# Performance work log

Measured on AMD Instinct MI355X. Metric: run time of the kernel, lower is better.

The kernel has to match this reference:

```python
import jax, jax.numpy as jnp
import numpy as np

# SOM hyperparameters (from init_kwargs)
M_ROWS = 64
N_COLS = 64
DIM = 256
MAX_EPOCHS = 100
INITIAL_RADIUS = 32.0  # max(m, n) / 2
INITIAL_LR = 0.1
STD_COEFF = 0.5
BATCH = 8192

# [m*n, 2] integer grid locations (constant, non-differentiable)
_LOC_VECTS = jnp.asarray(
    np.stack(np.meshgrid(np.arange(M_ROWS), np.arange(N_COLS), indexing='ij'), axis=-1).reshape(-1, 2),
    dtype=jnp.int32,
)


def setup_inputs() -> dict:
    key = jax.random.key(0)
    k1, k2 = jax.random.split(key)
    return {
        'input_vect': jax.random.normal(k1, (BATCH, DIM), dtype=jnp.float32),
        'weights': jax.random.normal(k2, (M_ROWS * N_COLS, DIM), dtype=jnp.float32),
        'epoch': 10,
    }


def reference(input_vect, weights, epoch):
    # squared_distance[b, m] = sum_d (weights[m, d] - x[b, d])^2  -> [B, M]
    sq_dist = (
        jnp.sum(input_vect * input_vect, axis=1, keepdims=True)
        - 2.0 * (input_vect @ weights.T)
        + jnp.sum(weights * weights, axis=1)[None, :]
    )
    bmu_indices = jnp.argmin(sq_dist, axis=1)             # [B]
    bmu_locs = _LOC_VECTS[bmu_indices]                    # [B, 2]

    ep = jnp.float32(epoch)
    radius = INITIAL_RADIUS - ep * ((INITIAL_RADIUS - 1.0) / (MAX_EPOCHS - 1.0))
    alpha = INITIAL_LR * (1.0 - ep / MAX_EPOCHS)

    # bmu_distance_squares[b, m] = ||locs[m] - bmu_locs[b]||^2  -> [B, M]
    diff = _LOC_VECTS[None, :, :] - bmu_locs[:, None, :]  # int [B, M, 2]
    bmu_dist_sq = jnp.sum(diff * diff, axis=2).astype(jnp.float32)

    denom_nf = 2.0 * jnp.square(radius * STD_COEFF)
    learning_rate_op = jnp.exp(-bmu_dist_sq / denom_nf) * alpha  # [B, M]

    # numerator[m, d] = sum_b lr[b, m] * x[b, d]
    numerator = jnp.einsum('bm,bd->md', learning_rate_op, input_vect)
    denominator = jnp.sum(learning_rate_op, axis=0)[:, None] + 1e-12  # [M, 1]
    new_weights = numerator / denominator
    return bmu_locs, new_weights
```

## Files before the change

### kernel.cpp

```cpp
#include <hip/hip_runtime.h>
#include <stdint.h>

#define DIM   256
#define BATCH 8192
#define MCELL 4096

typedef unsigned long long u64;
typedef unsigned short u16;
typedef __attribute__((ext_vector_type(8))) short bf16x8;
typedef __attribute__((ext_vector_type(4))) float f32x4;

__device__ __forceinline__ u64 packMin(float v, unsigned idx) {
    unsigned u = __float_as_uint(v);
    u = (u & 0x80000000u) ? ~u : (u | 0x80000000u);
    return ((u64)u << 32) | (u64)idx;
}
__device__ __forceinline__ u16 f2bf(float f) {
    unsigned u = __float_as_uint(f);
    u += 0x7fffu + ((u >> 16) & 1u);
    return (u16)(u >> 16);
}
__device__ __forceinline__ void gll16(const void* g, const char* l) {
    __builtin_amdgcn_global_load_lds(
        (const __attribute__((address_space(1))) unsigned int*)g,
        (__attribute__((address_space(3))) unsigned int*)l, 16, 0, 0);
}
__device__ __forceinline__ u64 umin64(u64 a, u64 b) { return a < b ? a : b; }
__device__ __forceinline__ u64 umax64(u64 a, u64 b) { return a < b ? b : a; }
__device__ __forceinline__ void ins2(u64& t1, u64& t2, u64 p) {
    u64 hi = umax64(p, t1);
    t1 = umin64(p, t1);
    t2 = umin64(t2, hi);
}
__device__ __forceinline__ void merge2(u64& a1, u64& a2, u64 o1, u64 o2) {
    u64 H1 = umax64(a1, o1);
    a1 = umin64(a1, o1);
    a2 = umin64(H1, umin64(a2, o2));
}
__device__ __forceinline__ void merge3(u64& a1, u64& a2, u64& a3,
                                       u64 o1, u64 o2, u64 o3) {
    u64 L1 = umin64(a1, o1), H1 = umax64(a1, o1);
    u64 L2 = umin64(a2, o2);
    u64 L3 = umin64(a3, o3);
    a1 = L1;
    a2 = umin64(H1, L2);
    a3 = umin64(umax64(H1, L2), L3);
}

__global__ void k_prep(const float* __restrict__ X, const float* __restrict__ W,
                       u16* __restrict__ Xh, u16* __restrict__ Wh,
                       float* __restrict__ w2, const int* __restrict__ epoch_p,
                       float* __restrict__ scal) {
    const int blk = blockIdx.x;
    const int t = threadIdx.x;
    if (blk == 3072) {
        int raw = epoch_p[0];
        float ep = (raw >= 0 && raw < 100000) ? (float)raw : __int_as_float(raw);
        float radius = 32.0f - ep * (31.0f / 99.0f);
        float alpha  = 0.1f * (1.0f - ep / 100.0f);
        float rs = radius * 0.5f;
        float denom = 2.0f * rs * rs;
        if (t < 64)       scal[t]  = expf(-((float)(t * t)) / denom);
        else if (t == 64) scal[64] = alpha;
        return;
    }
    if (blk < 2048) {
        const int fi = blk * 256 + t;
        float4 v = ((const float4*)X)[fi];
        ushort4 h = {f2bf(v.x), f2bf(v.y), f2bf(v.z), f2bf(v.w)};
        ((ushort4*)Xh)[fi] = h;
    } else {
        const int fi = (blk - 2048) * 256 + t;
        float4 v = ((const float4*)W)[fi];
        ushort4 h = {f2bf(v.x), f2bf(v.y), f2bf(v.z), f2bf(v.w)};
        ((ushort4*)Wh)[fi] = h;
        float s = v.x * v.x + v.y * v.y + v.z * v.z + v.w * v.w;
        #pragma unroll
        for (int off = 32; off; off >>= 1) s += __shfl_down(s, off);
        if ((t & 63) == 0) w2[fi >> 6] = s;
    }
}

__global__ __launch_bounds__(256, 3)
void k_gemm_argmin(const u16* __restrict__ Xh, const u16* __restrict__ Wh,
                   const float* __restrict__ w2, u64* __restrict__ slots) {
    __shared__ char smem[49152];
    const int wg = blockIdx.x;
    const int swz = (wg & 7) * 256 + (wg >> 3);
    const int bt = swz >> 5;
    const int mt = swz & 31;
    const int tid = threadIdx.x;
    const int wid = tid >> 6;
    const int lane = tid & 63;
    const int wr = wid >> 1, wc = wid & 1;
    const int b0 = bt * 128, m0 = mt * 128;

    const int sr0 = wid * 32 + (lane >> 2);
    const int sr1 = sr0 + 16;
    const int ss  = lane & 3;
    const int sg0 = ss ^ ((sr0 >> 1) & 3);
    const int sg1 = ss ^ ((sr1 >> 1) & 3);
    const size_t gA0 = (size_t)(b0 + sr0) * DIM + sg0 * 8;
    const size_t gA1 = (size_t)(b0 + sr1) * DIM + sg1 * 8;
    const size_t gB0 = (size_t)(m0 + sr0) * DIM + sg0 * 8;
    const size_t gB1 = (size_t)(m0 + sr1) * DIM + sg1 * 8;
    const int ldsA = wid * 2048;

    const int rl = lane & 15, g = lane >> 4;
    const int slot = g ^ ((rl >> 1) & 3);
    const int xoff = (wc * 64 + rl) * 64 + slot * 16;
    const int woff = (wr * 64 + rl) * 64 + slot * 16;

    f32x4 acc[4][4];
    #pragma unroll
    for (int i = 0; i < 4; ++i)
        #pragma unroll
        for (int j = 0; j < 4; ++j) acc[i][j] = (f32x4){0.f, 0.f, 0.f, 0.f};

    #define STAGE(buf, c) do {                                                \
        char* base_ = smem + (buf) * 16384;                                   \
        const int co_ = (c) * 32;                                             \
        gll16(Xh + gA0 + co_, base_ + ldsA);                                  \
        gll16(Xh + gA1 + co_, base_ + ldsA + 1024);                           \
        gll16(Wh + gB0 + co_, base_ + 8192 + ldsA);                           \
        gll16(Wh + gB1 + co_, base_ + 8192 + ldsA + 1024);                    \
    } while (0)

    STAGE(0, 0);
    STAGE(1, 1);
    #pragma unroll
    for (int c = 0; c < 8; ++c) {
        if (c < 6) {
            STAGE((c + 2) % 3, c + 2);
            asm volatile("s_waitcnt vmcnt(8)" ::: "memory");
        } else if (c == 6) {
            asm volatile("s_waitcnt vmcnt(4)" ::: "memory");
        } else {
            asm volatile("s_waitcnt vmcnt(0)" ::: "memory");
        }
        __builtin_amdgcn_sched_barrier(0);
        __builtin_amdgcn_s_barrier();

        const char* bufc = smem + (c % 3) * 16384;
        bf16x8 wf[4];
        #pragma unroll
        for (int i = 0; i < 4; ++i)
            wf[i] = *(const bf16x8*)(bufc + 8192 + woff + i * 1024);
        __builtin_amdgcn_s_setprio(1);
        #pragma unroll
        for (int j = 0; j < 4; ++j) {
            const bf16x8 xf = *(const bf16x8*)(bufc + xoff + j * 1024);
            #pragma unroll
            for (int i = 0; i < 4; ++i)
                acc[i][j] = __builtin_amdgcn_mfma_f32_16x16x32_bf16(wf[i], xf, acc[i][j], 0, 0, 0);
        }
        __builtin_amdgcn_s_setprio(0);
        __builtin_amdgcn_s_barrier();
    }
    #undef STAGE

    float w2v[16];
    #pragma unroll
    for (int ii = 0; ii < 16; ++ii)
        w2v[ii] = w2[m0 + wr * 64 + (ii >> 2) * 16 + g * 4 + (ii & 3)];

    __syncthreads();
    u64* ex = (u64*)smem;

    #pragma unroll
    for (int j = 0; j < 4; ++j) {
        u64 t1 = ~0ull, t2 = ~0ull;
        #pragma unroll
        for (int i = 0; i < 4; ++i)
            #pragma unroll
            for (int q = 0; q < 4; ++q) {
                const float d = fmaf(-2.0f, acc[i][j][q], w2v[i * 4 + q]);
                ins2(t1, t2, packMin(d, (unsigned)(m0 + wr * 64 + i * 16 + g * 4 + q)));
            }
        #pragma unroll
        for (int off = 16; off <= 32; off <<= 1) {
            const u64 o1 = __shfl_xor(t1, off);
            const u64 o2 = __shfl_xor(t2, off);
            merge2(t1, t2, o1, o2);
        }
        if (lane < 16) {
            u64* e = ex + ((size_t)(wc * 64 + j * 16 + rl) * 2 + wr) * 2;
            e[0] = t1; e[1] = t2;
        }
    }
    __syncthreads();
    if (tid < 128) {
        const u64* e = ex + (size_t)tid * 4;
        u64 a1 = e[0], a2 = e[1];
        merge2(a1, a2, e[2], e[3]);
        slots[(size_t)(b0 + tid) * 64 + mt]      = a1;
        slots[(size_t)(b0 + tid) * 64 + 32 + mt] = a2;
    }
}

__global__ void k_merge(const u64* __restrict__ slots, const float* __restrict__ X,
                        const float* __restrict__ W, const float* __restrict__ w2,
                        float* __restrict__ out_locs, int* __restrict__ bmu) {
    const int wid = threadIdx.x >> 6, l = threadIdx.x & 63;
    const int row = blockIdx.x * 4 + wid;
    u64 t1 = slots[(size_t)row * 64 + l], t2 = ~0ull, t3 = ~0ull;
    #pragma unroll
    for (int off = 1; off <= 32; off <<= 1) {
        const u64 o1 = __shfl_xor(t1, off);
        const u64 o2 = __shfl_xor(t2, off);
        const u64 o3 = __shfl_xor(t3, off);
        merge3(t1, t2, t3, o1, o2, o3);
    }
    const int cand[3] = {(int)(t1 & 0xFFFFFFFFull), (int)(t2 & 0xFFFFFFFFull),
                         (int)(t3 & 0xFFFFFFFFull)};
    const float4 xv = *(const float4*)(X + (size_t)row * DIM + l * 4);
    float bd = 0.0f; int bm = -1;
    #pragma unroll
    for (int tix = 0; tix < 3; ++tix) {
        const int mc = cand[tix];
        const float4 wv = *(const float4*)(W + (size_t)mc * DIM + l * 4);
        float s = xv.x * wv.x + xv.y * wv.y + xv.z * wv.z + xv.w * wv.w;
        #pragma unroll
        for (int off = 1; off <= 32; off <<= 1) s += __shfl_xor(s, off);
        const float d = w2[mc] - 2.0f * s;
        if (bm < 0 || d < bd || (d == bd && mc < bm)) { bd = d; bm = mc; }
    }
    if (l == 0) {
        out_locs[row * 2 + 0] = (float)(bm >> 6);
        out_locs[row * 2 + 1] = (float)(bm & 63);
        bmu[row] = bm;
    }
}

__global__ void k_gather(const int* __restrict__ bmu, const float* __restrict__ X,
                         float* __restrict__ A, float* __restrict__ cnt) {
    __shared__ int n;
    __shared__ int lst[BATCH];
    const int m = blockIdx.x;
    const int t = threadIdx.x;
    if (t == 0) n = 0;
    __syncthreads();
    #pragma unroll
    for (int i = 0; i < BATCH / 256; ++i) {
        const int r = i * 256 + t;
        if (bmu[r] == m) lst[atomicAdd(&n, 1)] = r;
    }
    __syncthreads();
    const int nn = n;
    float acc = 0.0f;
    for (int k = 0; k < nn; ++k)
        acc += X[(size_t)lst[k] * DIM + t];
    A[(size_t)m * DIM + t] = acc;
    if (t == 0) cnt[m] = (float)nn;
}

__global__ void k_conv1(const float* __restrict__ A, const float* __restrict__ E,
                        float* __restrict__ T1, const float* __restrict__ cnt,
                        float* __restrict__ c1) {
    if (blockIdx.x >= 4096) {
        int t = (blockIdx.x - 4096) * 256 + threadIdx.x;
        int gi = t >> 6, mj = t & 63;
        float acc = 0.0f;
        #pragma unroll
        for (int gj = 0; gj < 64; ++gj) {
            int dd = mj - gj; dd = dd < 0 ? -dd : dd;
            acc += E[dd] * cnt[gi * 64 + gj];
        }
        c1[gi * 64 + mj] = acc;
        return;
    }
    __shared__ float Es[64];
    const int d = threadIdx.x;
    if (d < 64) Es[d] = E[d];
    __syncthreads();
    const int gi = blockIdx.x >> 6, mj = blockIdx.x & 63;
    const float* base = A + (size_t)gi * 64 * DIM + d;
    float acc = 0.0f;
    #pragma unroll
    for (int gj = 0; gj < 64; ++gj) {
        int dd = mj - gj; dd = dd < 0 ? -dd : dd;
        acc += Es[dd] * base[(size_t)gj * DIM];
    }
    T1[(size_t)blockIdx.x * DIM + d] = acc;
}

__global__ void k_conv2(const float* __restrict__ T1, const float* __restrict__ scal,
                        const float* __restrict__ c1, float* __restrict__ outw) {
    __shared__ float Es[64];
    __shared__ float salpha;
    const int d = threadIdx.x;
    if (d < 64) Es[d] = scal[d];
    if (d == 64) salpha = scal[64];
    __syncthreads();
    const int mi = blockIdx.x >> 6, mj = blockIdx.x & 63;
    float acc = 0.0f, den = 0.0f;
    #pragma unroll
    for (int gi = 0; gi < 64; ++gi) {
        int dd = mi - gi; dd = dd < 0 ? -dd : dd;
        acc += Es[dd] * T1[((size_t)gi * 64 + mj) * DIM + d];
        den += Es[dd] * c1[gi * 64 + mj];
    }
    const float a = salpha;
    const float v = (a * acc) / (a * den + 1e-12f);
    outw[((size_t)mi * 64 + mj) * DIM + d] = v;
}

extern "C" void kernel_launch(void* const* d_in, const int* in_sizes, int n_in,
                              void* d_out, int out_size, void* d_ws, size_t ws_size,
                              hipStream_t stream) {
    const float* X = (const float*)d_in[0];
    const float* W = (const float*)d_in[1];
    const int*   ep = (const int*)d_in[2];
    float* out = (float*)d_out;

    char* ws = (char*)d_ws;
    u64*   slots = (u64*)(ws + 0);
    float* T1    = (float*)(ws + 0);
    u16*   Xh    = (u16*)(ws + (4u << 20));
    float* A     = (float*)(ws + (4u << 20));
    float* cnt   = (float*)(ws + (8u << 20));
    u16*   Wh    = (u16*)(ws + (8u << 20) + 16384);
    float* w2    = (float*)(ws + (10u << 20) + 16384);
    float* scal  = (float*)(ws + (10u << 20) + 32768);
    float* c1    = (float*)(ws + (10u << 20) + 36864);
    int*   bmu   = (int*)(ws + (10u << 20) + 53248);

    k_prep<<<3073, 256, 0, stream>>>(X, W, Xh, Wh, w2, ep, scal);
    k_gemm_argmin<<<2048, 256, 0, stream>>>(Xh, Wh, w2, slots);
    k_merge<<<2048, 256, 0, stream>>>(slots, X, W, w2, out, bmu);
    k_gather<<<MCELL, 256, 0, stream>>>(bmu, X, A, cnt);
    k_conv1<<<4112, 256, 0, stream>>>(A, scal, T1, cnt, c1);
    k_conv2<<<4096, 256, 0, stream>>>(T1, scal, c1, out + 16384);
}
```

Before: 163.1 us.

## Use per-wave private LDS staging in GEMM and register-blocked separable convolutions

New measurement: 185.9 us. 1.14x slower.

```diff
diff --git a/kernel.cpp b/kernel.cpp
--- a/kernel.cpp
+++ b/kernel.cpp
@@ -81,10 +81,10 @@
     }
 }
 
-__global__ __launch_bounds__(256, 3)
+__global__ __launch_bounds__(256, 2)
 void k_gemm_argmin(const u16* __restrict__ Xh, const u16* __restrict__ Wh,
                    const float* __restrict__ w2, u64* __restrict__ slots) {
-    __shared__ char smem[49152];
+    __shared__ char smem[65536];
     const int wg = blockIdx.x;
     const int swz = (wg & 7) * 256 + (wg >> 3);
     const int bt = swz >> 5;
@@ -94,22 +94,11 @@
     const int lane = tid & 63;
     const int wr = wid >> 1, wc = wid & 1;
     const int b0 = bt * 128, m0 = mt * 128;
-
-    const int sr0 = wid * 32 + (lane >> 2);
-    const int sr1 = sr0 + 16;
-    const int ss  = lane & 3;
-    const int sg0 = ss ^ ((sr0 >> 1) & 3);
-    const int sg1 = ss ^ ((sr1 >> 1) & 3);
-    const size_t gA0 = (size_t)(b0 + sr0) * DIM + sg0 * 8;
-    const size_t gA1 = (size_t)(b0 + sr1) * DIM + sg1 * 8;
-    const size_t gB0 = (size_t)(m0 + sr0) * DIM + sg0 * 8;
-    const size_t gB1 = (size_t)(m0 + sr1) * DIM + sg1 * 8;
-    const int ldsA = wid * 2048;
-
     const int rl = lane & 15, g = lane >> 4;
-    const int slot = g ^ ((rl >> 1) & 3);
-    const int xoff = (wc * 64 + rl) * 64 + slot * 16;
-    const int woff = (wr * 64 + rl) * 64 + slot * 16;
+
+    const u16* wsrc = Wh + (size_t)(m0 + wr * 64 + rl) * DIM + g * 8;
+    const u16* xsrc = Xh + (size_t)(b0 + wc * 64 + rl) * DIM + g * 8;
+    char* wb = smem + wid * 16384;
 
     f32x4 acc[4][4];
     #pragma unroll
@@ -118,44 +107,42 @@
         for (int j = 0; j < 4; ++j) acc[i][j] = (f32x4){0.f, 0.f, 0.f, 0.f};
 
     #define STAGE(buf, c) do {                                                \
-        char* base_ = smem + (buf) * 16384;                                   \
+        char* B_ = wb + (buf) * 8192;                                         \
         const int co_ = (c) * 32;                                             \
-        gll16(Xh + gA0 + co_, base_ + ldsA);                                  \
-        gll16(Xh + gA1 + co_, base_ + ldsA + 1024);                           \
-        gll16(Wh + gB0 + co_, base_ + 8192 + ldsA);                           \
-        gll16(Wh + gB1 + co_, base_ + 8192 + ldsA + 1024);                    \
+        gll16(wsrc + (size_t)0 * 16 * DIM + co_, B_ + 0 * 1024);              \
+        gll16(wsrc + (size_t)1 * 16 * DIM + co_, B_ + 1 * 1024);              \
+        gll16(wsrc + (size_t)2 * 16 * DIM + co_, B_ + 2 * 1024);              \
+        gll16(wsrc + (size_t)3 * 16 * DIM + co_, B_ + 3 * 1024);              \
+        gll16(xsrc + (size_t)0 * 16 * DIM + co_, B_ + 4 * 1024);              \
+        gll16(xsrc + (size_t)1 * 16 * DIM + co_, B_ + 5 * 1024);              \
+        gll16(xsrc + (size_t)2 * 16 * DIM + co_, B_ + 6 * 1024);              \
+        gll16(xsrc + (size_t)3 * 16 * DIM + co_, B_ + 7 * 1024);              \
     } while (0)
 
     STAGE(0, 0);
-    STAGE(1, 1);
     #pragma unroll
     for (int c = 0; c < 8; ++c) {
-        if (c < 6) {
-            STAGE((c + 2) % 3, c + 2);
+        if (c < 7) {
+            STAGE((c + 1) & 1, c + 1);
             asm volatile("s_waitcnt vmcnt(8)" ::: "memory");
-        } else if (c == 6) {
-            asm volatile("s_waitcnt vmcnt(4)" ::: "memory");
         } else {
             asm volatile("s_waitcnt vmcnt(0)" ::: "memory");
         }
         __builtin_amdgcn_sched_barrier(0);
-        __builtin_amdgcn_s_barrier();
-
-        const char* bufc = smem + (c % 3) * 16384;
+        const char* bufc = wb + (c & 1) * 8192 + lane * 16;
         bf16x8 wf[4];
         #pragma unroll
         for (int i = 0; i < 4; ++i)
-            wf[i] = *(const bf16x8*)(bufc + 8192 + woff + i * 1024);
+            wf[i] = *(const bf16x8*)(bufc + i * 1024);
         __builtin_amdgcn_s_setprio(1);
         #pragma unroll
         for (int j = 0; j < 4; ++j) {
-            const bf16x8 xf = *(const bf16x8*)(bufc + xoff + j * 1024);
+            const bf16x8 xf = *(const bf16x8*)(bufc + (4 + j) * 1024);
             #pragma unroll
             for (int i = 0; i < 4; ++i)
                 acc[i][j] = __builtin_amdgcn_mfma_f32_16x16x32_bf16(wf[i], xf, acc[i][j], 0, 0, 0);
         }
         __builtin_amdgcn_s_setprio(0);
-        __builtin_amdgcn_s_barrier();
     }
     #undef STAGE
 
@@ -235,7 +222,7 @@
 __global__ void k_gather(const int* __restrict__ bmu, const float* __restrict__ X,
                          float* __restrict__ A, float* __restrict__ cnt) {
     __shared__ int n;
-    __shared__ int lst[BATCH];
+    __shared__ u16 lst[BATCH];
     const int m = blockIdx.x;
     const int t = threadIdx.x;
     if (t == 0) n = 0;
@@ -243,7 +230,7 @@
     #pragma unroll
     for (int i = 0; i < BATCH / 256; ++i) {
         const int r = i * 256 + t;
-        if (bmu[r] == m) lst[atomicAdd(&n, 1)] = r;
+        if (bmu[r] == m) lst[atomicAdd(&n, 1)] = (u16)r;
     }
     __syncthreads();
     const int nn = n;
@@ -254,55 +241,110 @@
     if (t == 0) cnt[m] = (float)nn;
 }
 
-__global__ void k_conv1(const float* __restrict__ A, const float* __restrict__ E,
+template<int MJQ>
+__device__ __forceinline__ void conv1_body(int gi, int t, const float* __restrict__ A,
+                                           const float* __restrict__ scal,
+                                           float* __restrict__ T1) {
+    float a[64];
+    #pragma unroll
+    for (int gj = 0; gj < 64; ++gj)
+        a[gj] = A[(size_t)(gi * 64 + gj) * DIM + t];
+    float acc[16];
+    #pragma unroll
+    for (int i = 0; i < 16; ++i) acc[i] = 0.0f;
+    #pragma unroll
+    for (int gj = 0; gj < 64; ++gj) {
+        #pragma unroll
+        for (int mjl = 0; mjl < 16; ++mjl) {
+            const int mj = MJQ * 16 + mjl;
+            const int dd = (mj >= gj) ? (mj - gj) : (gj - mj);
+            acc[mjl] = fmaf(scal[dd], a[gj], acc[mjl]);
+        }
+    }
+    #pragma unroll
+    for (int mjl = 0; mjl < 16; ++mjl)
+        T1[(size_t)(gi * 64 + MJQ * 16 + mjl) * DIM + t] = acc[mjl];
+}
+
+__global__ void k_conv1(const float* __restrict__ A, const float* __restrict__ scal,
                         float* __restrict__ T1, const float* __restrict__ cnt,
                         float* __restrict__ c1) {
-    if (blockIdx.x >= 4096) {
-        int t = (blockIdx.x - 4096) * 256 + threadIdx.x;
-        int gi = t >> 6, mj = t & 63;
-        float acc = 0.0f;
-        #pragma unroll
-        for (int gj = 0; gj < 64; ++gj) {
-            int dd = mj - gj; dd = dd < 0 ? -dd : dd;
-            acc += E[dd] * cnt[gi * 64 + gj];
-        }
-        c1[gi * 64 + mj] = acc;
+    const int t = threadIdx.x;
+    if (blockIdx.x == 64) {
+        #pragma unroll
+        for (int k = 0; k < 4; ++k) {
+            const int o = blockIdx.y * 1024 + k * 256 + t;
+            const int gi = o >> 6, mj = o & 63;
+            float acc = 0.0f;
+            #pragma unroll
+            for (int gj = 0; gj < 64; ++gj) {
+                int dd = mj - gj; dd = dd < 0 ? -dd : dd;
+                acc += scal[dd] * cnt[gi * 64 + gj];
+            }
+            c1[o] = acc;
+        }
         return;
     }
-    __shared__ float Es[64];
-    const int d = threadIdx.x;
-    if (d < 64) Es[d] = E[d];
-    __syncthreads();
-    const int gi = blockIdx.x >> 6, mj = blockIdx.x & 63;
-    const float* base = A + (size_t)gi * 64 * DIM + d;
-    float acc = 0.0f;
-    #pragma unroll
-    for (int gj = 0; gj < 64; ++gj) {
-        int dd = mj - gj; dd = dd < 0 ? -dd : dd;
-        acc += Es[dd] * base[(size_t)gj * DIM];
-    }
-    T1[(size_t)blockIdx.x * DIM + d] = acc;
+    const int gi = blockIdx.x;
+    switch (blockIdx.y) {
+        case 0: conv1_body<0>(gi, t, A, scal, T1); break;
+        case 1: conv1_body<1>(gi, t, A, scal, T1); break;
+        case 2: conv1_body<2>(gi, t, A, scal, T1); break;
+        default: conv1_body<3>(gi, t, A, scal, T1); break;
+    }
+}
+
+template<int MIQ>
+__device__ __forceinline__ void conv2_body(int mj, int t, const float* __restrict__ T1,
+                                           const float* __restrict__ scal,
+                                           const float* __restrict__ c1,
+                                           float* __restrict__ outw) {
+    float t1r[64];
+    #pragma unroll
+    for (int gi = 0; gi < 64; ++gi)
+        t1r[gi] = T1[(size_t)(gi * 64 + mj) * DIM + t];
+    __shared__ float dens[16];
+    if (t < 16) {
+        const int mi = MIQ * 16 + t;
+        float dn = 0.0f;
+        #pragma unroll
+        for (int gi = 0; gi < 64; ++gi) {
+            int dd = mi - gi; dd = dd < 0 ? -dd : dd;
+            dn = fmaf(scal[dd], c1[gi * 64 + mj], dn);
+        }
+        dens[t] = dn;
+    }
+    __syncthreads();
+    float acc[16];
+    #pragma unroll
+    for (int i = 0; i < 16; ++i) acc[i] = 0.0f;
+    #pragma unroll
+    for (int gi = 0; gi < 64; ++gi) {
+        #pragma unroll
+        for (int mil = 0; mil < 16; ++mil) {
+            const int mi = MIQ * 16 + mil;
+            const int dd = (mi >= gi) ? (mi - gi) : (gi - mi);
+            acc[mil] = fmaf(scal[dd], t1r[gi], acc[mil]);
+        }
+    }
+    const float al = scal[64];
+    #pragma unroll
+    for (int mil = 0; mil < 16; ++mil) {
+        const int mi = MIQ * 16 + mil;
+        outw[(size_t)(mi * 64 + mj) * DIM + t] = (al * acc[mil]) / (al * dens[mil] + 1e-12f);
+    }
 }
 
 __global__ void k_conv2(const float* __restrict__ T1, const float* __restrict__ scal,
                         const float* __restrict__ c1, float* __restrict__ outw) {
-    __shared__ float Es[64];
-    __shared__ float salpha;
-    const int d = threadIdx.x;
-    if (d < 64) Es[d] = scal[d];
-    if (d == 64) salpha = scal[64];
-    __syncthreads();
-    const int mi = blockIdx.x >> 6, mj = blockIdx.x & 63;
-    float acc = 0.0f, den = 0.0f;
-    #pragma unroll
-    for (int gi = 0; gi < 64; ++gi) {
-        int dd = mi - gi; dd = dd < 0 ? -dd : dd;
-        acc += Es[dd] * T1[((size_t)gi * 64 + mj) * DIM + d];
-        den += Es[dd] * c1[gi * 64 + mj];
-    }
-    const float a = salpha;
-    const float v = (a * acc) / (a * den + 1e-12f);
-    outw[((size_t)mi * 64 + mj) * DIM + d] = v;
+    const int t = threadIdx.x;
+    const int mj = blockIdx.x;
+    switch (blockIdx.y) {
+        case 0: conv2_body<0>(mj, t, T1, scal, c1, outw); break;
+        case 1: conv2_body<1>(mj, t, T1, scal, c1, outw); break;
+        case 2: conv2_body<2>(mj, t, T1, scal, c1, outw); break;
+        default: conv2_body<3>(mj, t, T1, scal, c1, outw); break;
+    }
 }
 
 extern "C" void kernel_launch(void* const* d_in, const int* in_sizes, int n_in,
@@ -329,6 +371,6 @@
     k_gemm_argmin<<<2048, 256, 0, stream>>>(Xh, Wh, w2, slots);
     k_merge<<<2048, 256, 0, stream>>>(slots, X, W, w2, out, bmu);
     k_gather<<<MCELL, 256, 0, stream>>>(bmu, X, A, cnt);
-    k_conv1<<<4112, 256, 0, stream>>>(A, scal, T1, cnt, c1);
-    k_conv2<<<4096, 256, 0, stream>>>(T1, scal, c1, out + 16384);
-}
+    k_conv1<<<dim3(65, 4), 256, 0, stream>>>(A, scal, T1, cnt, c1);
+    k_conv2<<<dim3(64, 4), 256, 0, stream>>>(T1, scal, c1, out + 16384);
+}
```
